# Kernel tuning notes

Hardware: AMD Instinct MI355X
Metric: run time of the kernel (lower is better)

The kernel has to match this reference:

```python
import jax, jax.numpy as jnp
import numpy as np

STRIDES = (8, 16, 32, 64, 128)
FEATURE_SHAPES = ((100, 100), (50, 50), (25, 25), (13, 13), (7, 7))
POS_SCALE = 0.2
NUM_CLASSES = 80
MAX_GT = 100
IMG = 800.0
ALPHA, GAMMA = 0.25, 2.0
EPS = 1e-6


def setup_inputs() -> dict:
    key = jax.random.key(0)
    k1, k2, k3, k4, k5 = jax.random.split(key, 5)
    B = 8
    total = sum(h * w for h, w in FEATURE_SHAPES)  # 13343
    cls_pred = jax.random.uniform(k1, (B, total, NUM_CLASSES), jnp.float32, 0.01, 0.99)
    regr_pred = jax.random.uniform(k2, (B, total, 4), jnp.float32, 0.0, 1.0)
    # valid gt boxes in image coords, zero-padded tail (trim_zeros semantics)
    cxy = jax.random.uniform(k3, (B, MAX_GT, 2), jnp.float32, 100.0, 700.0)
    wh = jax.random.uniform(k4, (B, MAX_GT, 2), jnp.float32, 32.0, 300.0)
    x1y1 = jnp.clip(cxy - wh / 2, 0.0, IMG - 2.0)
    x2y2 = jnp.clip(cxy + wh / 2, x1y1 + 2.0, IMG)
    labels = jax.random.randint(k5, (B, MAX_GT, 1), 0, NUM_CLASSES).astype(jnp.float32)
    gt_boxes = jnp.concatenate([x1y1, x2y2, labels], axis=-1)
    valid = (jnp.arange(MAX_GT) < 70).astype(jnp.float32)[None, :, None]
    gt_boxes = gt_boxes * valid
    feature_shapes = jnp.array(FEATURE_SHAPES, jnp.int32)[None]
    return {"cls_pred": cls_pred, "regr_pred": regr_pred,
            "feature_shapes": feature_shapes, "gt_boxes": gt_boxes}


def _level_losses(cls_pred, regr_pred, boxes, labels):
    """cls_pred (T,C) sigmoid probs, regr_pred (T,4), boxes (N,4) xyxy, labels (N,) int32.
    Returns (N, num_levels) loss per gt box per FPN level. Replaces the original
    dynamic-slice-per-box tf.map_fn with padded rectangular masks per box."""
    out = []
    start = 0
    for (fh, fw), stride in zip(FEATURE_SHAPES, STRIDES):
        L = fh * fw
        cp = jnp.clip(cls_pred[start:start + L], EPS, 1.0 - EPS)  # (L,C)
        rp = regr_pred[start:start + L]                           # (L,4)
        start += L
        # focal loss: one-hot target => all-negative sum per location,
        # then swap the gt-label column from negative to positive term.
        neg = (1.0 - ALPHA) * cp ** GAMMA * (-jnp.log(1.0 - cp))  # (L,C)
        s_neg = neg.sum(-1)                                       # (L,)
        p_lab = cp[:, labels].T                                   # (N,L) gather at gt label
        neg_lab = (1.0 - ALPHA) * p_lab ** GAMMA * (-jnp.log(1.0 - p_lab))
        pos_lab = ALPHA * (1.0 - p_lab) ** GAMMA * (-jnp.log(p_lab))
        cls_loc = s_neg[None, :] - neg_lab + pos_lab              # (N,L)
        # prop_box_graph: shrink projected box by pos_scale around center
        pb = boxes / stride
        cx, cy = (pb[:, 0] + pb[:, 2]) / 2, (pb[:, 1] + pb[:, 3]) / 2
        hw = (pb[:, 2] - pb[:, 0]) * POS_SCALE / 2
        hh = (pb[:, 3] - pb[:, 1]) * POS_SCALE / 2
        x1 = jnp.clip(jnp.floor(cx - hw), 0, fw - 1).astype(jnp.int32)
        y1 = jnp.clip(jnp.floor(cy - hh), 0, fh - 1).astype(jnp.int32)
        x2 = jnp.clip(jnp.ceil(cx + hw).astype(jnp.int32), x1 + 1, fw)
        y2 = jnp.clip(jnp.ceil(cy + hh).astype(jnp.int32), y1 + 1, fh)
        yy, xx = jnp.meshgrid(jnp.arange(fh), jnp.arange(fw), indexing="ij")
        xx, yy = xx.reshape(-1), yy.reshape(-1)                   # (L,) row-major = flat idx
        mask = ((xx[None] >= x1[:, None]) & (xx[None] < x2[:, None]) &
                (yy[None] >= y1[:, None]) & (yy[None] < y2[:, None]))  # (N,L)
        cnt = jnp.maximum(mask.sum(-1), 1).astype(cls_pred.dtype)
        loss_cls = (cls_loc * mask).sum(-1) / cnt
        # iou loss on ltrb targets (shifted grid centers, /4 as in original)
        sx = (xx.astype(cls_pred.dtype) + 0.5) * stride
        sy = (yy.astype(cls_pred.dtype) + 0.5) * stride
        tl = (sx[None] - boxes[:, 0:1]) / 4.0                     # (N,L)
        tt = (sy[None] - boxes[:, 1:2]) / 4.0
        tr = (boxes[:, 2:3] - sx[None]) / 4.0
        tb = (boxes[:, 3:4] - sy[None]) / 4.0
        pl, pt, pr, pbm = rp[:, 0], rp[:, 1], rp[:, 2], rp[:, 3]
        t_area = (tl + tr) * (tt + tb)
        p_area = ((pl + pr) * (pt + pbm))[None]
        wi = jnp.minimum(pl[None], tl) + jnp.minimum(pr[None], tr)
        hi = jnp.minimum(pt[None], tt) + jnp.minimum(pbm[None], tb)
        ai = wi * hi
        union = t_area + p_area - ai
        iou_loc = -jnp.log((ai + 1.0) / (union + 1.0))            # (N,L)
        loss_regr = (iou_loc * mask).sum(-1) / cnt
        out.append(loss_cls + loss_regr)
    return jnp.stack(out, -1)  # (N, num_levels)


def _losses_batched(cls_pred, regr_pred, gt_boxes):
    labels = gt_boxes[..., 4].astype(jnp.int32)
    boxes = gt_boxes[..., :4]
    return jax.vmap(_level_losses)(cls_pred, regr_pred, boxes, labels)


def reference(cls_pred, regr_pred, feature_shapes, gt_boxes):
    # feature_shapes must be static under jit; FEATURE_SHAPES is the static copy,
    # the tensor arg is kept only for interface parity with the keras layer.
    losses = _losses_batched(cls_pred, regr_pred, gt_boxes)  # (B, MAX_GT, 5)
    levels = jnp.argmin(losses, axis=-1).astype(jnp.int32)
    valid = jnp.abs(gt_boxes[..., :4]).sum(-1) > 0           # trim_zeros_graph mask
    return jnp.where(valid, levels, -1)
```

## Files before the change

### kernel.cpp

```cpp
#include <hip/hip_runtime.h>
#include <math.h>


#define NCLS   80
#define NLEV   5
#define MAXGT  100
#define TOTAL  13343
#define BLK    256
#define CSPLIT 5

__device__ __forceinline__ float fadd(float a, float b) { return __fadd_rn(a, b); }
__device__ __forceinline__ float fsub(float a, float b) { return __fsub_rn(a, b); }
__device__ __forceinline__ float fmul(float a, float b) { return __fmul_rn(a, b); }
__device__ __forceinline__ float fdv (float a, float b) { return __fdiv_rn(a, b); }

struct Rect { int x1, y1, w, cells; };

__device__ __forceinline__ Rect mkrect(float b0, float b1, float b2, float b3,
                                       float st, int fd) {
    const float pb0 = fdv(b0, st), pb1 = fdv(b1, st);
    const float pb2 = fdv(b2, st), pb3 = fdv(b3, st);
    const float cx = fdv(fadd(pb0, pb2), 2.0f);
    const float cy = fdv(fadd(pb1, pb3), 2.0f);
    const float hw = fdv(fmul(fsub(pb2, pb0), 0.2f), 2.0f);
    const float hh = fdv(fmul(fsub(pb3, pb1), 0.2f), 2.0f);
    const int x1 = (int)fminf(fmaxf(floorf(fsub(cx, hw)), 0.0f), (float)(fd - 1));
    const int y1 = (int)fminf(fmaxf(floorf(fsub(cy, hh)), 0.0f), (float)(fd - 1));
    const int x2 = min(max((int)ceilf(fadd(cx, hw)), x1 + 1), fd);
    const int y2 = min(max((int)ceilf(fadd(cy, hh)), y1 + 1), fd);
    Rect r; r.x1 = x1; r.y1 = y1; r.w = x2 - x1; r.cells = (x2 - x1) * (y2 - y1);
    return r;
}

__device__ __forceinline__ double focal4(float4 v) {
    double s = 0.0;
    {
        const float cp = fminf(fmaxf(v.x, 1e-6f), 1.0f - 1e-6f);
        s += (double)(0.75f * cp * cp * (-logf(1.0f - cp)));
    }
    {
        const float cp = fminf(fmaxf(v.y, 1e-6f), 1.0f - 1e-6f);
        s += (double)(0.75f * cp * cp * (-logf(1.0f - cp)));
    }
    {
        const float cp = fminf(fmaxf(v.z, 1e-6f), 1.0f - 1e-6f);
        s += (double)(0.75f * cp * cp * (-logf(1.0f - cp)));
    }
    {
        const float cp = fminf(fmaxf(v.w, 1e-6f), 1.0f - 1e-6f);
        s += (double)(0.75f * cp * cp * (-logf(1.0f - cp)));
    }
    return s;
}

__device__ __forceinline__ double waveSumD(double v) {
    #pragma unroll
    for (int o = 32; o > 0; o >>= 1) v += __shfl_down(v, o, 64);
    return v;
}

__global__ __launch_bounds__(BLK) void level_select_kernel(
    const float* __restrict__ cls_pred,
    const float* __restrict__ regr_pred,
    const float* __restrict__ gt_boxes,
    int* __restrict__ out)
{
    const int bn  = blockIdx.x;
    const int b   = bn / MAXGT;
    const int tid = threadIdx.x;

    const float* box = gt_boxes + (size_t)bn * 5;
    const float b0 = box[0], b1 = box[1], b2 = box[2], b3 = box[3];
    const float vsum = fabsf(b0) + fabsf(b1) + fabsf(b2) + fabsf(b3);
    if (!(vsum > 0.0f)) {
        if (tid == 0) out[bn] = -1;
        return;
    }
    const int label = (int)box[4];

    const float* clsB = cls_pred  + (size_t)b * TOTAL * NCLS;
    const float* rgB  = regr_pred + (size_t)b * TOTAL * 4;

    const Rect r0 = mkrect(b0, b1, b2, b3,   8.0f, 100);
    const Rect r1 = mkrect(b0, b1, b2, b3,  16.0f,  50);
    const Rect r2 = mkrect(b0, b1, b2, b3,  32.0f,  25);
    const Rect r3 = mkrect(b0, b1, b2, b3,  64.0f,  13);
    const Rect r4 = mkrect(b0, b1, b2, b3, 128.0f,   7);

    const int woff1 = r0.cells * CSPLIT;
    const int woff2 = woff1 + r1.cells * CSPLIT;
    const int woff3 = woff2 + r2.cells * CSPLIT;
    const int woff4 = woff3 + r3.cells * CSPLIT;
    const int total = woff4 + r4.cells * CSPLIT;

    double a0 = 0.0, a1 = 0.0, a2 = 0.0, a3 = 0.0, a4 = 0.0;

    for (int wk = tid; wk < total; wk += BLK) {
        const int l = (wk >= woff1) + (wk >= woff2) + (wk >= woff3) + (wk >= woff4);

        const int base = (l == 0) ? 0 : (l == 1) ? woff1 : (l == 2) ? woff2
                       : (l == 3) ? woff3 : woff4;
        const Rect  rr    = (l == 0) ? r0 : (l == 1) ? r1 : (l == 2) ? r2
                          : (l == 3) ? r3 : r4;
        const float st    = (l == 0) ? 8.0f : (l == 1) ? 16.0f : (l == 2) ? 32.0f
                          : (l == 3) ? 64.0f : 128.0f;
        const int   fw    = (l == 0) ? 100 : (l == 1) ? 50 : (l == 2) ? 25
                          : (l == 3) ? 13 : 7;
        const int   start = (l == 0) ? 0 : (l == 1) ? 10000 : (l == 2) ? 12500
                          : (l == 3) ? 13125 : 13294;

        const int rel  = wk - base;
        const int cell = rel / CSPLIT;
        const int part = rel - cell * CSPLIT;
        const int cy   = cell / rr.w;
        const int x    = rr.x1 + (cell - cy * rr.w);
        const int y    = rr.y1 + cy;
        const int p    = start + y * fw + x;

        const float4* crow = (const float4*)(clsB + (size_t)p * NCLS + part * 16);
        double val = focal4(crow[0]) + focal4(crow[1]) + focal4(crow[2]) + focal4(crow[3]);

        if (part == 0) {
            const float plab = fminf(fmaxf(clsB[(size_t)p * NCLS + label], 1e-6f),
                                     1.0f - 1e-6f);
            const float neg_lab = 0.75f * plab * plab * (-logf(1.0f - plab));
            const float one_m   = 1.0f - plab;
            const float pos_lab = 0.25f * one_m * one_m * (-logf(plab));
            val += (double)pos_lab - (double)neg_lab;

            const float4 rp = *(const float4*)(rgB + (size_t)p * 4);
            const float sx = fmul(fadd((float)x, 0.5f), st);
            const float sy = fmul(fadd((float)y, 0.5f), st);
            const float tl = fdv(fsub(sx, b0), 4.0f);
            const float tt = fdv(fsub(sy, b1), 4.0f);
            const float tr = fdv(fsub(b2, sx), 4.0f);
            const float tb = fdv(fsub(b3, sy), 4.0f);
            const float t_area = fmul(fadd(tl, tr), fadd(tt, tb));
            const float p_area = fmul(fadd(rp.x, rp.z), fadd(rp.y, rp.w));
            const float wi = fadd(fminf(rp.x, tl), fminf(rp.z, tr));
            const float hi = fadd(fminf(rp.y, tt), fminf(rp.w, tb));
            const float ai = fmul(wi, hi);
            const float num = fadd(ai, 1.0f);
            const float den = fadd(fsub(fadd(t_area, p_area), ai), 1.0f);
            val += (double)(-logf(fdv(num, den)));
        }

        a0 += (l == 0) ? val : 0.0;
        a1 += (l == 1) ? val : 0.0;
        a2 += (l == 2) ? val : 0.0;
        a3 += (l == 3) ? val : 0.0;
        a4 += (l == 4) ? val : 0.0;
    }

    a0 = waveSumD(a0); a1 = waveSumD(a1); a2 = waveSumD(a2);
    a3 = waveSumD(a3); a4 = waveSumD(a4);

    __shared__ double s_red[BLK / 64][NLEV];
    const int wave = tid >> 6, lane = tid & 63;
    if (lane == 0) {
        s_red[wave][0] = a0; s_red[wave][1] = a1; s_red[wave][2] = a2;
        s_red[wave][3] = a3; s_red[wave][4] = a4;
    }
    __syncthreads();

    if (tid == 0) {
        double lv[NLEV];
        const int cellsArr[NLEV] = {r0.cells, r1.cells, r2.cells, r3.cells, r4.cells};
        #pragma unroll
        for (int l = 0; l < NLEV; ++l) {
            double t = 0.0;
            #pragma unroll
            for (int w = 0; w < BLK / 64; ++w) t += s_red[w][l];
            lv[l] = t / (double)cellsArr[l];
        }
        double best = INFINITY;
        int    idx  = 0;
        bool   accNan = false;
        #pragma unroll
        for (int l = 0; l < NLEV; ++l) {
            const double v = lv[l];
            if (!accNan && (isnan(v) || v < best)) {
                best = v; idx = l; accNan = isnan(v);
            }
        }
        out[bn] = idx;
    }
}

extern "C" void kernel_launch(void* const* d_in, const int* in_sizes, int n_in,
                              void* d_out, int out_size, void* d_ws, size_t ws_size,
                              hipStream_t stream) {
    (void)d_ws; (void)ws_size; (void)out_size;
    const float* cls_pred  = (const float*)d_in[0];
    const float* regr_pred = (const float*)d_in[1];
    const float* gt_boxes  = (const float*)d_in[3];
    for (int i = 0; i < n_in; ++i) {
        if      (in_sizes[i] == 8 * TOTAL * NCLS) cls_pred  = (const float*)d_in[i];
        else if (in_sizes[i] == 8 * TOTAL * 4)    regr_pred = (const float*)d_in[i];
        else if (in_sizes[i] == 8 * MAXGT * 5)    gt_boxes  = (const float*)d_in[i];
    }
    int* out = (int*)d_out;

    level_select_kernel<<<8 * MAXGT, BLK, 0, stream>>>(cls_pred, regr_pred, gt_boxes, out);
}
```

Baseline: 89.26 us.

## Precompute per-location negative focal sums once in a separate pass

Adds a first kernel that computes the 80-class negative focal sum for every location once and stores it in the workspace as doubles. The per-box kernel then reads that sum instead of recomputing it for every overlapping box, and drops to one wave per block with no shared-memory reduction. This removes redundant transcendental work on cells shared by many boxes. In exchange it reads the full class tensor once and adds a second launch plus a workspace dependency.

```diff
diff --git a/kernel.cpp b/kernel.cpp
--- a/kernel.cpp
+++ b/kernel.cpp
@@ -6,13 +6,53 @@
 #define NLEV   5
 #define MAXGT  100
 #define TOTAL  13343
-#define BLK    256
-#define CSPLIT 5
+#define NROWS  (8 * TOTAL)
 
 __device__ __forceinline__ float fadd(float a, float b) { return __fadd_rn(a, b); }
 __device__ __forceinline__ float fsub(float a, float b) { return __fsub_rn(a, b); }
 __device__ __forceinline__ float fmul(float a, float b) { return __fmul_rn(a, b); }
 __device__ __forceinline__ float fdv (float a, float b) { return __fdiv_rn(a, b); }
+
+__device__ __forceinline__ double focal4(float4 v) {
+    double s = 0.0;
+    {
+        const float cp = fminf(fmaxf(v.x, 1e-6f), 1.0f - 1e-6f);
+        s += (double)(0.75f * cp * cp * (-logf(1.0f - cp)));
+    }
+    {
+        const float cp = fminf(fmaxf(v.y, 1e-6f), 1.0f - 1e-6f);
+        s += (double)(0.75f * cp * cp * (-logf(1.0f - cp)));
+    }
+    {
+        const float cp = fminf(fmaxf(v.z, 1e-6f), 1.0f - 1e-6f);
+        s += (double)(0.75f * cp * cp * (-logf(1.0f - cp)));
+    }
+    {
+        const float cp = fminf(fmaxf(v.w, 1e-6f), 1.0f - 1e-6f);
+        s += (double)(0.75f * cp * cp * (-logf(1.0f - cp)));
+    }
+    return s;
+}
+
+__global__ __launch_bounds__(256) void sneg_kernel(
+    const float* __restrict__ cls_pred,
+    double* __restrict__ sneg)
+{
+    const int t   = blockIdx.x * 256 + threadIdx.x;
+    const int row = t >> 2;
+    const int sub = t & 3;
+    if (row >= NROWS) return;
+
+    const float4* rp = (const float4*)(cls_pred + (size_t)row * NCLS) + sub;
+    double s = 0.0;
+    #pragma unroll
+    for (int j = 0; j < 5; ++j)
+        s += focal4(rp[j * 4]);
+
+    s += __shfl_xor(s, 1, 64);
+    s += __shfl_xor(s, 2, 64);
+    if (sub == 0) sneg[row] = s;
+}
 
 struct Rect { int x1, y1, w, cells; };
 
@@ -32,37 +72,17 @@
     return r;
 }
 
-__device__ __forceinline__ double focal4(float4 v) {
-    double s = 0.0;
-    {
-        const float cp = fminf(fmaxf(v.x, 1e-6f), 1.0f - 1e-6f);
-        s += (double)(0.75f * cp * cp * (-logf(1.0f - cp)));
-    }
-    {
-        const float cp = fminf(fmaxf(v.y, 1e-6f), 1.0f - 1e-6f);
-        s += (double)(0.75f * cp * cp * (-logf(1.0f - cp)));
-    }
-    {
-        const float cp = fminf(fmaxf(v.z, 1e-6f), 1.0f - 1e-6f);
-        s += (double)(0.75f * cp * cp * (-logf(1.0f - cp)));
-    }
-    {
-        const float cp = fminf(fmaxf(v.w, 1e-6f), 1.0f - 1e-6f);
-        s += (double)(0.75f * cp * cp * (-logf(1.0f - cp)));
-    }
-    return s;
-}
-
 __device__ __forceinline__ double waveSumD(double v) {
     #pragma unroll
     for (int o = 32; o > 0; o >>= 1) v += __shfl_down(v, o, 64);
     return v;
 }
 
-__global__ __launch_bounds__(BLK) void level_select_kernel(
+__global__ __launch_bounds__(64) void level_select_kernel(
     const float* __restrict__ cls_pred,
     const float* __restrict__ regr_pred,
     const float* __restrict__ gt_boxes,
+    const double* __restrict__ sneg,
     int* __restrict__ out)
 {
     const int bn  = blockIdx.x;
@@ -78,8 +98,9 @@
     }
     const int label = (int)box[4];
 
-    const float* clsB = cls_pred  + (size_t)b * TOTAL * NCLS;
-    const float* rgB  = regr_pred + (size_t)b * TOTAL * 4;
+    const float*  clsB  = cls_pred + (size_t)b * TOTAL * NCLS;
+    const float*  rgB   = regr_pred + (size_t)b * TOTAL * 4;
+    const double* snegB = sneg + (size_t)b * TOTAL;
 
     const Rect r0 = mkrect(b0, b1, b2, b3,   8.0f, 100);
     const Rect r1 = mkrect(b0, b1, b2, b3,  16.0f,  50);
@@ -87,19 +108,19 @@
     const Rect r3 = mkrect(b0, b1, b2, b3,  64.0f,  13);
     const Rect r4 = mkrect(b0, b1, b2, b3, 128.0f,   7);
 
-    const int woff1 = r0.cells * CSPLIT;
-    const int woff2 = woff1 + r1.cells * CSPLIT;
-    const int woff3 = woff2 + r2.cells * CSPLIT;
-    const int woff4 = woff3 + r3.cells * CSPLIT;
-    const int total = woff4 + r4.cells * CSPLIT;
+    const int o1 = r0.cells;
+    const int o2 = o1 + r1.cells;
+    const int o3 = o2 + r2.cells;
+    const int o4 = o3 + r3.cells;
+    const int total = o4 + r4.cells;
 
     double a0 = 0.0, a1 = 0.0, a2 = 0.0, a3 = 0.0, a4 = 0.0;
 
-    for (int wk = tid; wk < total; wk += BLK) {
-        const int l = (wk >= woff1) + (wk >= woff2) + (wk >= woff3) + (wk >= woff4);
-
-        const int base = (l == 0) ? 0 : (l == 1) ? woff1 : (l == 2) ? woff2
-                       : (l == 3) ? woff3 : woff4;
+    for (int c = tid; c < total; c += 64) {
+        const int l = (c >= o1) + (c >= o2) + (c >= o3) + (c >= o4);
+
+        const int base = (l == 0) ? 0 : (l == 1) ? o1 : (l == 2) ? o2
+                       : (l == 3) ? o3 : o4;
         const Rect  rr    = (l == 0) ? r0 : (l == 1) ? r1 : (l == 2) ? r2
                           : (l == 3) ? r3 : r4;
         const float st    = (l == 0) ? 8.0f : (l == 1) ? 16.0f : (l == 2) ? 32.0f
@@ -109,41 +130,36 @@
         const int   start = (l == 0) ? 0 : (l == 1) ? 10000 : (l == 2) ? 12500
                           : (l == 3) ? 13125 : 13294;
 
-        const int rel  = wk - base;
-        const int cell = rel / CSPLIT;
-        const int part = rel - cell * CSPLIT;
-        const int cy   = cell / rr.w;
-        const int x    = rr.x1 + (cell - cy * rr.w);
-        const int y    = rr.y1 + cy;
-        const int p    = start + y * fw + x;
-
-        const float4* crow = (const float4*)(clsB + (size_t)p * NCLS + part * 16);
-        double val = focal4(crow[0]) + focal4(crow[1]) + focal4(crow[2]) + focal4(crow[3]);
-
-        if (part == 0) {
-            const float plab = fminf(fmaxf(clsB[(size_t)p * NCLS + label], 1e-6f),
-                                     1.0f - 1e-6f);
-            const float neg_lab = 0.75f * plab * plab * (-logf(1.0f - plab));
-            const float one_m   = 1.0f - plab;
-            const float pos_lab = 0.25f * one_m * one_m * (-logf(plab));
-            val += (double)pos_lab - (double)neg_lab;
-
-            const float4 rp = *(const float4*)(rgB + (size_t)p * 4);
-            const float sx = fmul(fadd((float)x, 0.5f), st);
-            const float sy = fmul(fadd((float)y, 0.5f), st);
-            const float tl = fdv(fsub(sx, b0), 4.0f);
-            const float tt = fdv(fsub(sy, b1), 4.0f);
-            const float tr = fdv(fsub(b2, sx), 4.0f);
-            const float tb = fdv(fsub(b3, sy), 4.0f);
-            const float t_area = fmul(fadd(tl, tr), fadd(tt, tb));
-            const float p_area = fmul(fadd(rp.x, rp.z), fadd(rp.y, rp.w));
-            const float wi = fadd(fminf(rp.x, tl), fminf(rp.z, tr));
-            const float hi = fadd(fminf(rp.y, tt), fminf(rp.w, tb));
-            const float ai = fmul(wi, hi);
-            const float num = fadd(ai, 1.0f);
-            const float den = fadd(fsub(fadd(t_area, p_area), ai), 1.0f);
-            val += (double)(-logf(fdv(num, den)));
-        }
+        const int rel = c - base;
+        const int cy  = rel / rr.w;
+        const int x   = rr.x1 + (rel - cy * rr.w);
+        const int y   = rr.y1 + cy;
+        const int p   = start + y * fw + x;
+
+        double val = snegB[p];
+
+        const float plab = fminf(fmaxf(clsB[(size_t)p * NCLS + label], 1e-6f),
+                                 1.0f - 1e-6f);
+        const float neg_lab = 0.75f * plab * plab * (-logf(1.0f - plab));
+        const float one_m   = 1.0f - plab;
+        const float pos_lab = 0.25f * one_m * one_m * (-logf(plab));
+        val += (double)pos_lab - (double)neg_lab;
+
+        const float4 rp = *(const float4*)(rgB + (size_t)p * 4);
+        const float sx = fmul(fadd((float)x, 0.5f), st);
+        const float sy = fmul(fadd((float)y, 0.5f), st);
+        const float tl = fdv(fsub(sx, b0), 4.0f);
+        const float tt = fdv(fsub(sy, b1), 4.0f);
+        const float tr = fdv(fsub(b2, sx), 4.0f);
+        const float tb = fdv(fsub(b3, sy), 4.0f);
+        const float t_area = fmul(fadd(tl, tr), fadd(tt, tb));
+        const float p_area = fmul(fadd(rp.x, rp.z), fadd(rp.y, rp.w));
+        const float wi = fadd(fminf(rp.x, tl), fminf(rp.z, tr));
+        const float hi = fadd(fminf(rp.y, tt), fminf(rp.w, tb));
+        const float ai = fmul(wi, hi);
+        const float num = fadd(ai, 1.0f);
+        const float den = fadd(fsub(fadd(t_area, p_area), ai), 1.0f);
+        val += (double)(-logf(fdv(num, den)));
 
         a0 += (l == 0) ? val : 0.0;
         a1 += (l == 1) ? val : 0.0;
@@ -155,24 +171,13 @@
     a0 = waveSumD(a0); a1 = waveSumD(a1); a2 = waveSumD(a2);
     a3 = waveSumD(a3); a4 = waveSumD(a4);
 
-    __shared__ double s_red[BLK / 64][NLEV];
-    const int wave = tid >> 6, lane = tid & 63;
-    if (lane == 0) {
-        s_red[wave][0] = a0; s_red[wave][1] = a1; s_red[wave][2] = a2;
-        s_red[wave][3] = a3; s_red[wave][4] = a4;
-    }
-    __syncthreads();
-
     if (tid == 0) {
         double lv[NLEV];
-        const int cellsArr[NLEV] = {r0.cells, r1.cells, r2.cells, r3.cells, r4.cells};
-        #pragma unroll
-        for (int l = 0; l < NLEV; ++l) {
-            double t = 0.0;
-            #pragma unroll
-            for (int w = 0; w < BLK / 64; ++w) t += s_red[w][l];
-            lv[l] = t / (double)cellsArr[l];
-        }
+        lv[0] = a0 / (double)r0.cells;
+        lv[1] = a1 / (double)r1.cells;
+        lv[2] = a2 / (double)r2.cells;
+        lv[3] = a3 / (double)r3.cells;
+        lv[4] = a4 / (double)r4.cells;
         double best = INFINITY;
         int    idx  = 0;
         bool   accNan = false;
@@ -190,7 +195,7 @@
 extern "C" void kernel_launch(void* const* d_in, const int* in_sizes, int n_in,
                               void* d_out, int out_size, void* d_ws, size_t ws_size,
                               hipStream_t stream) {
-    (void)d_ws; (void)ws_size; (void)out_size;
+    (void)out_size;
     const float* cls_pred  = (const float*)d_in[0];
     const float* regr_pred = (const float*)d_in[1];
     const float* gt_boxes  = (const float*)d_in[3];
@@ -200,6 +205,13 @@
         else if (in_sizes[i] == 8 * MAXGT * 5)    gt_boxes  = (const float*)d_in[i];
     }
     int* out = (int*)d_out;
-
-    level_select_kernel<<<8 * MAXGT, BLK, 0, stream>>>(cls_pred, regr_pred, gt_boxes, out);
-}
+    double* sneg = (double*)d_ws;
+    (void)ws_size;
+
+    const int k1_threads = NROWS * 4;
+    const int k1_blocks  = (k1_threads + 255) / 256;
+    sneg_kernel<<<k1_blocks, 256, 0, stream>>>(cls_pred, sneg);
+
+    level_select_kernel<<<8 * MAXGT, 64, 0, stream>>>(
+        cls_pred, regr_pred, gt_boxes, sneg, out);
+}
```

New measurement: 86.53 us. -3.1%, faster.
